# Optimization experiments

Measured on AMD Instinct MI355X. Metric: run time of the kernel, lower is better.

## Reference

```python
import jax, jax.numpy as jnp
import numpy as np

N_NODES = 100000
N_EDGES = 1600000
D = 64
N_LAYERS = 6  # 3 KAN blocks x 2 KANLinear
GRID_SIZE = 5
SPLINE_ORDER = 3
N_COEF = GRID_SIZE + SPLINE_ORDER  # 8


def _grid():
    # uniform B-spline grid on [-1, 1], extended by spline_order on each side
    h = 2.0 / GRID_SIZE
    return (jnp.arange(-SPLINE_ORDER, GRID_SIZE + SPLINE_ORDER + 1, dtype=jnp.float32) * h - 1.0)  # [G+2k+1]=12


def b_splines(x):
    # x: [N, D] -> bases [N, D, G+k] via Cox-de Boor recursion
    grid = _grid()
    xe = x[..., None]  # [N, D, 1]
    b = ((xe >= grid[:-1]) & (xe < grid[1:])).astype(x.dtype)  # order-0, [N,D,G+2k]
    for p in range(1, SPLINE_ORDER + 1):
        left = (xe - grid[: -(p + 1)]) / (grid[p:-1] - grid[: -(p + 1)])
        right = (grid[p + 1:] - xe) / (grid[p + 1:] - grid[1:-p])
        b = left * b[..., :-1] + right * b[..., 1:]
    return b  # [N, D, N_COEF]


def kan_linear(x, bw, sw, ss):
    # efficient-KAN layer: SiLU base branch + B-spline branch with standalone scaler
    base = jax.nn.silu(x) @ bw.T                      # [N, O]
    bas = b_splines(x)                                # [N, D, K]
    spline = jnp.einsum('ndk,odk->no', bas, sw * ss[..., None])
    return base + spline


def spmm(edge_row, edge_col, edge_val, x):
    # out[i] = sum_{(i,j) in E} val * x[j]  -- COO sparse-dense matmul
    msgs = edge_val[:, None] * x[edge_col]            # [E, D] gather
    return jax.ops.segment_sum(msgs, edge_row, num_segments=N_NODES)


def setup_inputs() -> dict:
    key = jax.random.key(0)
    ks = jax.random.split(key, 7)
    x = jax.random.uniform(ks[0], (N_NODES, D), jnp.float32, -1.0, 1.0)
    edge_row = jnp.sort(jax.random.randint(ks[1], (N_EDGES,), 0, N_NODES))
    edge_col = jax.random.randint(ks[2], (N_EDGES,), 0, N_NODES)
    edge_val = jax.random.uniform(ks[3], (N_EDGES,), jnp.float32, 0.0, 1.0) * (1.0 / 16.0)
    base_w = jax.random.normal(ks[4], (N_LAYERS, D, D), jnp.float32) * (1.0 / np.sqrt(D))
    spline_w = jax.random.normal(ks[5], (N_LAYERS, D, D, N_COEF), jnp.float32) * 0.1
    spline_s = jax.random.normal(ks[6], (N_LAYERS, D, D), jnp.float32) * (1.0 / np.sqrt(D))
    return {"x": x, "edge_val": edge_val, "base_w": base_w, "spline_w": spline_w,
            "spline_s": spline_s, "edge_row": edge_row, "edge_col": edge_col}


def reference(x, edge_val, base_w, spline_w, spline_s, edge_row, edge_col):
    idx = 0
    for _block in range(3):          # mp_layers = 3 KAN blocks
        x = spmm(edge_row, edge_col, edge_val, x)
        for _l in range(2):          # kan_layers = 2 KANLinear per block
            x = kan_linear(x, base_w[idx], spline_w[idx], spline_s[idx])
            idx += 1
    return x
```

## Files before the change

kernel.cpp:

```cpp
#include <hip/hip_runtime.h>
#include <math.h>

#define N_NODES 100000
#define N_EDGES 1600000
#define DIM 64
#define N_LAYERS 6
#define N_COEF 8
#define NSTEP 18
#define NTILE 32
#define KAN_BLOCKS (N_NODES / NTILE)

typedef _Float16 f16x8 __attribute__((ext_vector_type(8)));
typedef _Float16 f16x4 __attribute__((ext_vector_type(4)));
typedef float f32x4 __attribute__((ext_vector_type(4)));

__device__ __forceinline__ unsigned f16u(float v) {
    return (unsigned)__builtin_bit_cast(unsigned short, (_Float16)v);
}

__global__ void build_wcf(const float* __restrict__ bw,
                          const float* __restrict__ sw,
                          const float* __restrict__ ss,
                          uint4* __restrict__ wcf) {
    int idx = blockIdx.x * blockDim.x + threadIdx.x;
    if (idx >= N_LAYERS * NSTEP * 4 * 64) return;
    int lane = idx & 63;
    int nt   = (idx >> 6) & 3;
    int s    = (idx >> 8) % NSTEP;
    int l    = idx / (64 * 4 * NSTEP);
    int o = nt * 16 + (lane & 15);

    unsigned short h[8];
#pragma unroll
    for (int j = 0; j < 8; ++j) {
        int k = s * 32 + ((lane >> 4) << 3) + j;
        int d = k / 9;
        int r = k - d * 9;
        float v;
        if (r == 0) v = bw[(l * DIM + o) * DIM + d];
        else        v = sw[((l * DIM + o) * DIM + d) * N_COEF + (r - 1)] *
                        ss[(l * DIM + o) * DIM + d];
        h[j] = __builtin_bit_cast(unsigned short, (_Float16)v);
    }
    uint4 uh;
    uh.x = (unsigned)h[0] | ((unsigned)h[1] << 16);
    uh.y = (unsigned)h[2] | ((unsigned)h[3] << 16);
    uh.z = (unsigned)h[4] | ((unsigned)h[5] << 16);
    uh.w = (unsigned)h[6] | ((unsigned)h[7] << 16);
    wcf[((l * NSTEP + s) * 4 + nt) * 64 + lane] = uh;
}

__global__ void build_rowptr(const int* __restrict__ erow, int* __restrict__ rp) {
    int i = blockIdx.x * blockDim.x + threadIdx.x;
    if (i > N_NODES) return;
    if (i == N_NODES) { rp[i] = N_EDGES; return; }
    int a = 0, b = N_EDGES;
    while (a < b) { int m = (a + b) >> 1; if (erow[m] < i) a = m + 1; else b = m; }
    rp[i] = a;
}

__global__ void conv_f16(const float* __restrict__ in, _Float16* __restrict__ out) {
    int i = blockIdx.x * blockDim.x + threadIdx.x;
    float4 v = *(const float4*)(in + (size_t)i * 4);
    f16x4 h = { (_Float16)v.x, (_Float16)v.y, (_Float16)v.z, (_Float16)v.w };
    *(f16x4*)(out + (size_t)i * 4) = h;
}

#define META16(C, V, BASE)                                              \
    _Pragma("unroll")                                                   \
    for (int i_ = 0; i_ < 4; ++i_) {                                    \
        int e_ = (BASE) + 4 * i_ + q;                                   \
        if (e_ < end) { C[i_] = ecol[e_]; V[i_] = ev[e_]; }             \
        else          { C[i_] = 0;        V[i_] = 0.f; }                \
    }

__global__ __launch_bounds__(256) void spmm_kernel(const int* __restrict__ rp,
                                                   const int* __restrict__ ecol,
                                                   const float* __restrict__ ev,
                                                   const _Float16* __restrict__ x,
                                                   _Float16* __restrict__ y) {
    int wid = (blockIdx.x * blockDim.x + threadIdx.x) >> 6;
    int lane = threadIdx.x & 63;
    if (wid >= N_NODES) return;
    int q = lane >> 4;
    int c16 = lane & 15;
    int e0 = rp[wid], end = rp[wid + 1];

    float4 acc = {0.f, 0.f, 0.f, 0.f};
    int ca[4]; float va[4];
    int cb[4]; float vb[4];
    META16(ca, va, e0)

    for (int eb = e0; eb < end; eb += 16) {
        META16(cb, vb, eb + 16)
        f16x4 g0 = *(const f16x4*)&x[(size_t)ca[0] * DIM + c16 * 4];
        f16x4 g1 = *(const f16x4*)&x[(size_t)ca[1] * DIM + c16 * 4];
        f16x4 g2 = *(const f16x4*)&x[(size_t)ca[2] * DIM + c16 * 4];
        f16x4 g3 = *(const f16x4*)&x[(size_t)ca[3] * DIM + c16 * 4];
        acc.x += va[0] * (float)g0[0]; acc.y += va[0] * (float)g0[1];
        acc.z += va[0] * (float)g0[2]; acc.w += va[0] * (float)g0[3];
        acc.x += va[1] * (float)g1[0]; acc.y += va[1] * (float)g1[1];
        acc.z += va[1] * (float)g1[2]; acc.w += va[1] * (float)g1[3];
        acc.x += va[2] * (float)g2[0]; acc.y += va[2] * (float)g2[1];
        acc.z += va[2] * (float)g2[2]; acc.w += va[2] * (float)g2[3];
        acc.x += va[3] * (float)g3[0]; acc.y += va[3] * (float)g3[1];
        acc.z += va[3] * (float)g3[2]; acc.w += va[3] * (float)g3[3];
#pragma unroll
        for (int i_ = 0; i_ < 4; ++i_) { ca[i_] = cb[i_]; va[i_] = vb[i_]; }
    }

    acc.x += __shfl_xor(acc.x, 16); acc.y += __shfl_xor(acc.y, 16);
    acc.z += __shfl_xor(acc.z, 16); acc.w += __shfl_xor(acc.w, 16);
    acc.x += __shfl_xor(acc.x, 32); acc.y += __shfl_xor(acc.y, 32);
    acc.z += __shfl_xor(acc.z, 32); acc.w += __shfl_xor(acc.w, 32);

    if (lane < 16) {
        f16x4 h = { (_Float16)acc.x, (_Float16)acc.y, (_Float16)acc.z, (_Float16)acc.w };
        *(f16x4*)&y[(size_t)wid * DIM + c16 * 4] = h;
    }
}

__device__ __forceinline__ void spline_window(float xv, unsigned long long& lo,
                                              unsigned long long& hi) {
    float t = xv * 2.5f + 5.5f;
    float fl = floorf(t);
    float u = t - fl;
    int c = (int)fl;
    bool valid = (t >= 0.f) && (t < 11.f);
    float u2 = u * u, u3 = u2 * u, um = 1.f - u;
    const float k6 = 1.f / 6.f;
    float N0 = um * um * um * k6;
    float N1 = (3.f * u3 - 6.f * u2 + 4.f) * k6;
    float N2 = (-3.f * u3 + 3.f * u2 + 3.f * u + 1.f) * k6;
    float N3 = u3 * k6;
    if (!valid) { N0 = 0.f; N1 = 0.f; N2 = 0.f; N3 = 0.f; }
    unsigned n01 = f16u(N0) | (f16u(N1) << 16);
    unsigned n23 = f16u(N2) | (f16u(N3) << 16);
    unsigned long long big = (unsigned long long)n01 | ((unsigned long long)n23 << 32);
    int qb = c - 3;
    qb = qb < -3 ? -3 : (qb > 7 ? 7 : qb);
    int sh = qb * 16;
    lo = 0; hi = 0;
    if (sh >= 0) {
        if (sh < 64) { lo = big << sh; hi = (big >> 1) >> (63 - sh); }
        else         { hi = big << (sh - 64); }
    } else {
        lo = big >> (-sh);
    }
}

__device__ __forceinline__ void feat_pair(char* lds, int lbase, int Xsw, int d,
                                          float xe, float xo) {
    float se_f = xe * __builtin_amdgcn_rcpf(1.f + __expf(-xe));
    float so_f = xo * __builtin_amdgcn_rcpf(1.f + __expf(-xo));
    unsigned se = f16u(se_f), so = f16u(so_f);

    unsigned long long loE, hiE, loO, hiO;
    spline_window(xe, loE, hiE);
    spline_window(xo, loO, hiO);

    unsigned wv[9];
    wv[0] = se | ((unsigned)loE << 16);
    wv[1] = (unsigned)(loE >> 16);
    wv[2] = (unsigned)(loE >> 48) | ((unsigned)hiE << 16);
    wv[3] = (unsigned)(hiE >> 16);
    wv[4] = (unsigned)(hiE >> 48) | (so << 16);
    wv[5] = (unsigned)loO;
    wv[6] = (unsigned)(loO >> 32);
    wv[7] = (unsigned)hiO;
    wv[8] = (unsigned)(hiO >> 32);

    int base = lbase + 18 * d;
#pragma unroll
    for (int j = 0; j < 9; ++j)
        *(unsigned*)(&lds[(base + 4 * j) ^ Xsw]) = wv[j];
}

template<int F32OUT>
__global__ __launch_bounds__(256) void kan_mfma(const _Float16* __restrict__ xin,
                                                const uint4* __restrict__ wl,
                                                void* __restrict__ outp) {
    __shared__ alignas(16) char lds[NTILE * 1152];

    int tid = threadIdx.x;
    int lane = tid & 63;
    int w = tid >> 6;
    int node0 = blockIdx.x * NTILE;

    int fn = tid >> 3;
    int fq = tid & 7;
    int Xsw = (fn & 7) << 4;
    int lbase = fn * 1152;
    {
        const _Float16* xr_ = &xin[(size_t)(node0 + fn) * DIM + fq * 4];
        f16x4 h0 = *(const f16x4*)(xr_);
        f16x4 h1 = *(const f16x4*)(xr_ + 32);
        int d0 = fq * 4;
        feat_pair(lds, lbase, Xsw, d0,          (float)h0[0], (float)h0[1]);
        feat_pair(lds, lbase, Xsw, d0 + 2,      (float)h0[2], (float)h0[3]);
        feat_pair(lds, lbase, Xsw, d0 + 32,     (float)h1[0], (float)h1[1]);
        feat_pair(lds, lbase, Xsw, d0 + 32 + 2, (float)h1[2], (float)h1[3]);
    }
    __syncthreads();

    int row = lane & 15, kg = lane >> 4;
    int xr = (row & 7) << 4;
    int rb0 = row * 1152;
    int rb1 = (16 + row) * 1152;

    f32x4 acc0 = {0.f, 0.f, 0.f, 0.f};
    f32x4 acc1 = {0.f, 0.f, 0.f, 0.f};
#pragma unroll
    for (int s = 0; s < NSTEP; ++s) {
        f16x8 bh = __builtin_bit_cast(f16x8, wl[(s * 4 + w) * 64 + lane]);
        int pofs = ((s * 4 + kg) << 4) ^ xr;
        f16x8 a0 = *(const f16x8*)(&lds[rb0 + pofs]);
        f16x8 a1 = *(const f16x8*)(&lds[rb1 + pofs]);
        acc0 = __builtin_amdgcn_mfma_f32_16x16x32_f16(a0, bh, acc0, 0, 0, 0);
        acc1 = __builtin_amdgcn_mfma_f32_16x16x32_f16(a1, bh, acc1, 0, 0, 0);
    }

    int o = w * 16 + row;
    int rbase = kg * 4;
    if (F32OUT) {
        float* out = (float*)outp;
#pragma unroll
        for (int r = 0; r < 4; ++r) {
            out[(size_t)(node0 + rbase + r) * DIM + o]      = acc0[r];
            out[(size_t)(node0 + 16 + rbase + r) * DIM + o] = acc1[r];
        }
    } else {
        _Float16* out = (_Float16*)outp;
#pragma unroll
        for (int r = 0; r < 4; ++r) {
            out[(size_t)(node0 + rbase + r) * DIM + o]      = (_Float16)acc0[r];
            out[(size_t)(node0 + 16 + rbase + r) * DIM + o] = (_Float16)acc1[r];
        }
    }
}

extern "C" void kernel_launch(void* const* d_in, const int* in_sizes, int n_in,
                              void* d_out, int out_size, void* d_ws, size_t ws_size,
                              hipStream_t stream) {
    const float* x     = (const float*)d_in[0];
    const float* eval_ = (const float*)d_in[1];
    const float* bw    = (const float*)d_in[2];
    const float* sw    = (const float*)d_in[3];
    const float* ss    = (const float*)d_in[4];
    const int*   erow  = (const int*)d_in[5];
    const int*   ecol  = (const int*)d_in[6];
    float* out = (float*)d_out;

    const size_t HB = (size_t)N_NODES * DIM * sizeof(_Float16);
    _Float16* H0 = (_Float16*)d_ws;
    _Float16* H1 = (_Float16*)((char*)d_ws + HB);
    uint4* wcf = (uint4*)((char*)d_ws + 2 * HB);
    int*   rp  = (int*)((char*)d_ws + 2 * HB + 442368);

    const size_t WL = (size_t)NSTEP * 4 * 64;

    build_wcf<<<(N_LAYERS * NSTEP * 4 * 64 + 255) / 256, 256, 0, stream>>>(bw, sw, ss, wcf);
    build_rowptr<<<(N_NODES + 256) / 256, 256, 0, stream>>>(erow, rp);
    conv_f16<<<(N_NODES * DIM / 4 + 255) / 256, 256, 0, stream>>>(x, H0);

    const int SPMM_BLOCKS = N_NODES / 4;

    spmm_kernel<<<SPMM_BLOCKS, 256, 0, stream>>>(rp, ecol, eval_, H0, H1);
    kan_mfma<0><<<KAN_BLOCKS, 256, 0, stream>>>(H1, wcf + 0 * WL, H1);
    kan_mfma<0><<<KAN_BLOCKS, 256, 0, stream>>>(H1, wcf + 1 * WL, H0);

    spmm_kernel<<<SPMM_BLOCKS, 256, 0, stream>>>(rp, ecol, eval_, H0, H1);
    kan_mfma<0><<<KAN_BLOCKS, 256, 0, stream>>>(H1, wcf + 2 * WL, H1);
    kan_mfma<0><<<KAN_BLOCKS, 256, 0, stream>>>(H1, wcf + 3 * WL, H0);

    spmm_kernel<<<SPMM_BLOCKS, 256, 0, stream>>>(rp, ecol, eval_, H0, H1);
    kan_mfma<0><<<KAN_BLOCKS, 256, 0, stream>>>(H1, wcf + 4 * WL, H1);
    kan_mfma<1><<<KAN_BLOCKS, 256, 0, stream>>>(H1, wcf + 5 * WL, out);
}
```

Before: 272.4 us.

## Double KAN node tile to 64, fuse prep kernels, use 32-bit gather indexing

Each KAN MFMA block now processes 64 nodes with four accumulators, so each weight fragment load is reused across more MFMAs, with bounds guards for the partial final tile. The three setup kernels are merged into one launch with block-range dispatch to cut launch overhead. The SpMM gather address is computed with an unsigned 32-bit shift to save 64-bit arithmetic. The larger LDS footprint per block reduces how many blocks can be resident per CU.

```diff
diff --git a/kernel.cpp b/kernel.cpp
--- a/kernel.cpp
+++ b/kernel.cpp
@@ -7,8 +7,12 @@
 #define N_LAYERS 6
 #define N_COEF 8
 #define NSTEP 18
-#define NTILE 32
+#define NTILE 64
 #define KAN_BLOCKS (N_NODES / NTILE)
+
+#define WCF_BLOCKS 108
+#define RP_BLOCKS  391
+#define CONV_BLOCKS 6250
 
 typedef _Float16 f16x8 __attribute__((ext_vector_type(8)));
 typedef _Float16 f16x4 __attribute__((ext_vector_type(4)));
@@ -18,52 +22,53 @@
     return (unsigned)__builtin_bit_cast(unsigned short, (_Float16)v);
 }
 
-__global__ void build_wcf(const float* __restrict__ bw,
-                          const float* __restrict__ sw,
-                          const float* __restrict__ ss,
-                          uint4* __restrict__ wcf) {
-    int idx = blockIdx.x * blockDim.x + threadIdx.x;
-    if (idx >= N_LAYERS * NSTEP * 4 * 64) return;
-    int lane = idx & 63;
-    int nt   = (idx >> 6) & 3;
-    int s    = (idx >> 8) % NSTEP;
-    int l    = idx / (64 * 4 * NSTEP);
-    int o = nt * 16 + (lane & 15);
-
-    unsigned short h[8];
-#pragma unroll
-    for (int j = 0; j < 8; ++j) {
-        int k = s * 32 + ((lane >> 4) << 3) + j;
-        int d = k / 9;
-        int r = k - d * 9;
-        float v;
-        if (r == 0) v = bw[(l * DIM + o) * DIM + d];
-        else        v = sw[((l * DIM + o) * DIM + d) * N_COEF + (r - 1)] *
-                        ss[(l * DIM + o) * DIM + d];
-        h[j] = __builtin_bit_cast(unsigned short, (_Float16)v);
-    }
-    uint4 uh;
-    uh.x = (unsigned)h[0] | ((unsigned)h[1] << 16);
-    uh.y = (unsigned)h[2] | ((unsigned)h[3] << 16);
-    uh.z = (unsigned)h[4] | ((unsigned)h[5] << 16);
-    uh.w = (unsigned)h[6] | ((unsigned)h[7] << 16);
-    wcf[((l * NSTEP + s) * 4 + nt) * 64 + lane] = uh;
-}
-
-__global__ void build_rowptr(const int* __restrict__ erow, int* __restrict__ rp) {
-    int i = blockIdx.x * blockDim.x + threadIdx.x;
-    if (i > N_NODES) return;
-    if (i == N_NODES) { rp[i] = N_EDGES; return; }
-    int a = 0, b = N_EDGES;
-    while (a < b) { int m = (a + b) >> 1; if (erow[m] < i) a = m + 1; else b = m; }
-    rp[i] = a;
-}
-
-__global__ void conv_f16(const float* __restrict__ in, _Float16* __restrict__ out) {
-    int i = blockIdx.x * blockDim.x + threadIdx.x;
-    float4 v = *(const float4*)(in + (size_t)i * 4);
-    f16x4 h = { (_Float16)v.x, (_Float16)v.y, (_Float16)v.z, (_Float16)v.w };
-    *(f16x4*)(out + (size_t)i * 4) = h;
+__global__ __launch_bounds__(256) void prep(const float* __restrict__ bw,
+                                            const float* __restrict__ sw,
+                                            const float* __restrict__ ss,
+                                            uint4* __restrict__ wcf,
+                                            const int* __restrict__ erow,
+                                            int* __restrict__ rp,
+                                            const float* __restrict__ x,
+                                            _Float16* __restrict__ H0) {
+    int bid = blockIdx.x;
+    if (bid < WCF_BLOCKS) {
+        int idx = bid * 256 + threadIdx.x;
+        int lane = idx & 63;
+        int nt   = (idx >> 6) & 3;
+        int s    = (idx >> 8) % NSTEP;
+        int l    = idx / (64 * 4 * NSTEP);
+        int o = nt * 16 + (lane & 15);
+        unsigned short h[8];
+#pragma unroll
+        for (int j = 0; j < 8; ++j) {
+            int k = s * 32 + ((lane >> 4) << 3) + j;
+            int d = k / 9;
+            int r = k - d * 9;
+            float v;
+            if (r == 0) v = bw[(l * DIM + o) * DIM + d];
+            else        v = sw[((l * DIM + o) * DIM + d) * N_COEF + (r - 1)] *
+                            ss[(l * DIM + o) * DIM + d];
+            h[j] = __builtin_bit_cast(unsigned short, (_Float16)v);
+        }
+        uint4 uh;
+        uh.x = (unsigned)h[0] | ((unsigned)h[1] << 16);
+        uh.y = (unsigned)h[2] | ((unsigned)h[3] << 16);
+        uh.z = (unsigned)h[4] | ((unsigned)h[5] << 16);
+        uh.w = (unsigned)h[6] | ((unsigned)h[7] << 16);
+        wcf[((l * NSTEP + s) * 4 + nt) * 64 + lane] = uh;
+    } else if (bid < WCF_BLOCKS + RP_BLOCKS) {
+        int i = (bid - WCF_BLOCKS) * 256 + threadIdx.x;
+        if (i > N_NODES) return;
+        if (i == N_NODES) { rp[i] = N_EDGES; return; }
+        int a = 0, b = N_EDGES;
+        while (a < b) { int m = (a + b) >> 1; if (erow[m] < i) a = m + 1; else b = m; }
+        rp[i] = a;
+    } else {
+        int i = (bid - WCF_BLOCKS - RP_BLOCKS) * 256 + threadIdx.x;
+        float4 v = *(const float4*)(x + (size_t)i * 4);
+        f16x4 h = { (_Float16)v.x, (_Float16)v.y, (_Float16)v.z, (_Float16)v.w };
+        *(f16x4*)(H0 + (size_t)i * 4) = h;
+    }
 }
 
 #define META16(C, V, BASE)                                              \
@@ -93,10 +98,10 @@
 
     for (int eb = e0; eb < end; eb += 16) {
         META16(cb, vb, eb + 16)
-        f16x4 g0 = *(const f16x4*)&x[(size_t)ca[0] * DIM + c16 * 4];
-        f16x4 g1 = *(const f16x4*)&x[(size_t)ca[1] * DIM + c16 * 4];
-        f16x4 g2 = *(const f16x4*)&x[(size_t)ca[2] * DIM + c16 * 4];
-        f16x4 g3 = *(const f16x4*)&x[(size_t)ca[3] * DIM + c16 * 4];
+        f16x4 g0 = *(const f16x4*)&x[((unsigned)ca[0] << 6) + c16 * 4];
+        f16x4 g1 = *(const f16x4*)&x[((unsigned)ca[1] << 6) + c16 * 4];
+        f16x4 g2 = *(const f16x4*)&x[((unsigned)ca[2] << 6) + c16 * 4];
+        f16x4 g3 = *(const f16x4*)&x[((unsigned)ca[3] << 6) + c16 * 4];
         acc.x += va[0] * (float)g0[0]; acc.y += va[0] * (float)g0[1];
         acc.z += va[0] * (float)g0[2]; acc.w += va[0] * (float)g0[3];
         acc.x += va[1] * (float)g1[0]; acc.y += va[1] * (float)g1[1];
@@ -187,54 +192,65 @@
     int w = tid >> 6;
     int node0 = blockIdx.x * NTILE;
 
-    int fn = tid >> 3;
-    int fq = tid & 7;
+    int fn = tid >> 2;
+    int fq = tid & 3;
+    bool live = (node0 + fn) < N_NODES;
     int Xsw = (fn & 7) << 4;
     int lbase = fn * 1152;
-    {
+    if (live) {
         const _Float16* xr_ = &xin[(size_t)(node0 + fn) * DIM + fq * 4];
-        f16x4 h0 = *(const f16x4*)(xr_);
-        f16x4 h1 = *(const f16x4*)(xr_ + 32);
-        int d0 = fq * 4;
-        feat_pair(lds, lbase, Xsw, d0,          (float)h0[0], (float)h0[1]);
-        feat_pair(lds, lbase, Xsw, d0 + 2,      (float)h0[2], (float)h0[3]);
-        feat_pair(lds, lbase, Xsw, d0 + 32,     (float)h1[0], (float)h1[1]);
-        feat_pair(lds, lbase, Xsw, d0 + 32 + 2, (float)h1[2], (float)h1[3]);
+#pragma unroll
+        for (int i = 0; i < 4; ++i) {
+            f16x4 h = *(const f16x4*)(xr_ + i * 16);
+            int d0 = fq * 4 + i * 16;
+            feat_pair(lds, lbase, Xsw, d0,     (float)h[0], (float)h[1]);
+            feat_pair(lds, lbase, Xsw, d0 + 2, (float)h[2], (float)h[3]);
+        }
     }
     __syncthreads();
 
     int row = lane & 15, kg = lane >> 4;
     int xr = (row & 7) << 4;
-    int rb0 = row * 1152;
-    int rb1 = (16 + row) * 1152;
+    int rb0 = (0 * 16 + row) * 1152;
+    int rb1 = (1 * 16 + row) * 1152;
+    int rb2 = (2 * 16 + row) * 1152;
+    int rb3 = (3 * 16 + row) * 1152;
 
     f32x4 acc0 = {0.f, 0.f, 0.f, 0.f};
     f32x4 acc1 = {0.f, 0.f, 0.f, 0.f};
+    f32x4 acc2 = {0.f, 0.f, 0.f, 0.f};
+    f32x4 acc3 = {0.f, 0.f, 0.f, 0.f};
 #pragma unroll
     for (int s = 0; s < NSTEP; ++s) {
         f16x8 bh = __builtin_bit_cast(f16x8, wl[(s * 4 + w) * 64 + lane]);
         int pofs = ((s * 4 + kg) << 4) ^ xr;
         f16x8 a0 = *(const f16x8*)(&lds[rb0 + pofs]);
         f16x8 a1 = *(const f16x8*)(&lds[rb1 + pofs]);
+        f16x8 a2 = *(const f16x8*)(&lds[rb2 + pofs]);
+        f16x8 a3 = *(const f16x8*)(&lds[rb3 + pofs]);
         acc0 = __builtin_amdgcn_mfma_f32_16x16x32_f16(a0, bh, acc0, 0, 0, 0);
         acc1 = __builtin_amdgcn_mfma_f32_16x16x32_f16(a1, bh, acc1, 0, 0, 0);
+        acc2 = __builtin_amdgcn_mfma_f32_16x16x32_f16(a2, bh, acc2, 0, 0, 0);
+        acc3 = __builtin_amdgcn_mfma_f32_16x16x32_f16(a3, bh, acc3, 0, 0, 0);
     }
 
     int o = w * 16 + row;
     int rbase = kg * 4;
-    if (F32OUT) {
-        float* out = (float*)outp;
-#pragma unroll
-        for (int r = 0; r < 4; ++r) {
-            out[(size_t)(node0 + rbase + r) * DIM + o]      = acc0[r];
-            out[(size_t)(node0 + 16 + rbase + r) * DIM + o] = acc1[r];
-        }
-    } else {
-        _Float16* out = (_Float16*)outp;
-#pragma unroll
-        for (int r = 0; r < 4; ++r) {
-            out[(size_t)(node0 + rbase + r) * DIM + o]      = (_Float16)acc0[r];
-            out[(size_t)(node0 + 16 + rbase + r) * DIM + o] = (_Float16)acc1[r];
+#pragma unroll
+    for (int m = 0; m < 4; ++m) {
+        f32x4 acc = m == 0 ? acc0 : m == 1 ? acc1 : m == 2 ? acc2 : acc3;
+        int nb = node0 + m * 16 + rbase;
+        if (nb >= N_NODES) continue;
+        if (F32OUT) {
+            float* out = (float*)outp;
+#pragma unroll
+            for (int r = 0; r < 4; ++r)
+                out[(size_t)(nb + r) * DIM + o] = acc[r];
+        } else {
+            _Float16* out = (_Float16*)outp;
+#pragma unroll
+            for (int r = 0; r < 4; ++r)
+                out[(size_t)(nb + r) * DIM + o] = (_Float16)acc[r];
         }
     }
 }
@@ -258,22 +274,22 @@
     int*   rp  = (int*)((char*)d_ws + 2 * HB + 442368);
 
     const size_t WL = (size_t)NSTEP * 4 * 64;
-
-    build_wcf<<<(N_LAYERS * NSTEP * 4 * 64 + 255) / 256, 256, 0, stream>>>(bw, sw, ss, wcf);
-    build_rowptr<<<(N_NODES + 256) / 256, 256, 0, stream>>>(erow, rp);
-    conv_f16<<<(N_NODES * DIM / 4 + 255) / 256, 256, 0, stream>>>(x, H0);
+    const int KB = (N_NODES + NTILE - 1) / NTILE;
+
+    prep<<<WCF_BLOCKS + RP_BLOCKS + CONV_BLOCKS, 256, 0, stream>>>(
+        bw, sw, ss, wcf, erow, rp, x, H0);
 
     const int SPMM_BLOCKS = N_NODES / 4;
 
     spmm_kernel<<<SPMM_BLOCKS, 256, 0, stream>>>(rp, ecol, eval_, H0, H1);
-    kan_mfma<0><<<KAN_BLOCKS, 256, 0, stream>>>(H1, wcf + 0 * WL, H1);
-    kan_mfma<0><<<KAN_BLOCKS, 256, 0, stream>>>(H1, wcf + 1 * WL, H0);
+    kan_mfma<0><<<KB, 256, 0, stream>>>(H1, wcf + 0 * WL, H1);
+    kan_mfma<0><<<KB, 256, 0, stream>>>(H1, wcf + 1 * WL, H0);
 
     spmm_kernel<<<SPMM_BLOCKS, 256, 0, stream>>>(rp, ecol, eval_, H0, H1);
-    kan_mfma<0><<<KAN_BLOCKS, 256, 0, stream>>>(H1, wcf + 2 * WL, H1);
-    kan_mfma<0><<<KAN_BLOCKS, 256, 0, stream>>>(H1, wcf + 3 * WL, H0);
+    kan_mfma<0><<<KB, 256, 0, stream>>>(H1, wcf + 2 * WL, H1);
+    kan_mfma<0><<<KB, 256, 0, stream>>>(H1, wcf + 3 * WL, H0);
 
     spmm_kernel<<<SPMM_BLOCKS, 256, 0, stream>>>(rp, ecol, eval_, H0, H1);
-    kan_mfma<0><<<KAN_BLOCKS, 256, 0, stream>>>(H1, wcf + 4 * WL, H1);
-    kan_mfma<1><<<KAN_BLOCKS, 256, 0, stream>>>(H1, wcf + 5 * WL, out);
-}
+    kan_mfma<0><<<KB, 256, 0, stream>>>(H1, wcf + 4 * WL, H1);
+    kan_mfma<1><<<KB, 256, 0, stream>>>(H1, wcf + 5 * WL, out);
+}
```

New measurement: 295.8 us. 1.09x slower.

## Fuse paired KAN layers into one kernel and merge prep kernels

Applied to the files above, without the earlier changes.

Each pair of consecutive KANLinear layers now runs in one kernel. The intermediate activations stay in LDS, where they are re-featurized for the second layer's MFMA loop, so the global round trip and one launch per block are removed. The three setup kernels are merged into a single prep launch with a block-range dispatch. The SpMM gather index arithmetic also switches to 32-bit shifts. The cost is extra syncthreads and LDS reuse inside the fused kernel.

```diff
diff --git a/kernel.cpp b/kernel.cpp
--- a/kernel.cpp
+++ b/kernel.cpp
@@ -9,6 +9,11 @@
 #define NSTEP 18
 #define NTILE 32
 #define KAN_BLOCKS (N_NODES / NTILE)
+#define C1S 68
+
+#define WCF_BLOCKS 108
+#define RP_BLOCKS  391
+#define CONV_BLOCKS 6250
 
 typedef _Float16 f16x8 __attribute__((ext_vector_type(8)));
 typedef _Float16 f16x4 __attribute__((ext_vector_type(4)));
@@ -18,52 +23,53 @@
     return (unsigned)__builtin_bit_cast(unsigned short, (_Float16)v);
 }
 
-__global__ void build_wcf(const float* __restrict__ bw,
-                          const float* __restrict__ sw,
-                          const float* __restrict__ ss,
-                          uint4* __restrict__ wcf) {
-    int idx = blockIdx.x * blockDim.x + threadIdx.x;
-    if (idx >= N_LAYERS * NSTEP * 4 * 64) return;
-    int lane = idx & 63;
-    int nt   = (idx >> 6) & 3;
-    int s    = (idx >> 8) % NSTEP;
-    int l    = idx / (64 * 4 * NSTEP);
-    int o = nt * 16 + (lane & 15);
-
-    unsigned short h[8];
-#pragma unroll
-    for (int j = 0; j < 8; ++j) {
-        int k = s * 32 + ((lane >> 4) << 3) + j;
-        int d = k / 9;
-        int r = k - d * 9;
-        float v;
-        if (r == 0) v = bw[(l * DIM + o) * DIM + d];
-        else        v = sw[((l * DIM + o) * DIM + d) * N_COEF + (r - 1)] *
-                        ss[(l * DIM + o) * DIM + d];
-        h[j] = __builtin_bit_cast(unsigned short, (_Float16)v);
-    }
-    uint4 uh;
-    uh.x = (unsigned)h[0] | ((unsigned)h[1] << 16);
-    uh.y = (unsigned)h[2] | ((unsigned)h[3] << 16);
-    uh.z = (unsigned)h[4] | ((unsigned)h[5] << 16);
-    uh.w = (unsigned)h[6] | ((unsigned)h[7] << 16);
-    wcf[((l * NSTEP + s) * 4 + nt) * 64 + lane] = uh;
-}
-
-__global__ void build_rowptr(const int* __restrict__ erow, int* __restrict__ rp) {
-    int i = blockIdx.x * blockDim.x + threadIdx.x;
-    if (i > N_NODES) return;
-    if (i == N_NODES) { rp[i] = N_EDGES; return; }
-    int a = 0, b = N_EDGES;
-    while (a < b) { int m = (a + b) >> 1; if (erow[m] < i) a = m + 1; else b = m; }
-    rp[i] = a;
-}
-
-__global__ void conv_f16(const float* __restrict__ in, _Float16* __restrict__ out) {
-    int i = blockIdx.x * blockDim.x + threadIdx.x;
-    float4 v = *(const float4*)(in + (size_t)i * 4);
-    f16x4 h = { (_Float16)v.x, (_Float16)v.y, (_Float16)v.z, (_Float16)v.w };
-    *(f16x4*)(out + (size_t)i * 4) = h;
+__global__ __launch_bounds__(256) void prep(const float* __restrict__ bw,
+                                            const float* __restrict__ sw,
+                                            const float* __restrict__ ss,
+                                            uint4* __restrict__ wcf,
+                                            const int* __restrict__ erow,
+                                            int* __restrict__ rp,
+                                            const float* __restrict__ x,
+                                            _Float16* __restrict__ H0) {
+    int bid = blockIdx.x;
+    if (bid < WCF_BLOCKS) {
+        int idx = bid * 256 + threadIdx.x;
+        int lane = idx & 63;
+        int nt   = (idx >> 6) & 3;
+        int s    = (idx >> 8) % NSTEP;
+        int l    = idx / (64 * 4 * NSTEP);
+        int o = nt * 16 + (lane & 15);
+        unsigned short h[8];
+#pragma unroll
+        for (int j = 0; j < 8; ++j) {
+            int k = s * 32 + ((lane >> 4) << 3) + j;
+            int d = k / 9;
+            int r = k - d * 9;
+            float v;
+            if (r == 0) v = bw[(l * DIM + o) * DIM + d];
+            else        v = sw[((l * DIM + o) * DIM + d) * N_COEF + (r - 1)] *
+                            ss[(l * DIM + o) * DIM + d];
+            h[j] = __builtin_bit_cast(unsigned short, (_Float16)v);
+        }
+        uint4 uh;
+        uh.x = (unsigned)h[0] | ((unsigned)h[1] << 16);
+        uh.y = (unsigned)h[2] | ((unsigned)h[3] << 16);
+        uh.z = (unsigned)h[4] | ((unsigned)h[5] << 16);
+        uh.w = (unsigned)h[6] | ((unsigned)h[7] << 16);
+        wcf[((l * NSTEP + s) * 4 + nt) * 64 + lane] = uh;
+    } else if (bid < WCF_BLOCKS + RP_BLOCKS) {
+        int i = (bid - WCF_BLOCKS) * 256 + threadIdx.x;
+        if (i > N_NODES) return;
+        if (i == N_NODES) { rp[i] = N_EDGES; return; }
+        int a = 0, b = N_EDGES;
+        while (a < b) { int m = (a + b) >> 1; if (erow[m] < i) a = m + 1; else b = m; }
+        rp[i] = a;
+    } else {
+        int i = (bid - WCF_BLOCKS - RP_BLOCKS) * 256 + threadIdx.x;
+        float4 v = *(const float4*)(x + (size_t)i * 4);
+        f16x4 h = { (_Float16)v.x, (_Float16)v.y, (_Float16)v.z, (_Float16)v.w };
+        *(f16x4*)(H0 + (size_t)i * 4) = h;
+    }
 }
 
 #define META16(C, V, BASE)                                              \
@@ -93,10 +99,10 @@
 
     for (int eb = e0; eb < end; eb += 16) {
         META16(cb, vb, eb + 16)
-        f16x4 g0 = *(const f16x4*)&x[(size_t)ca[0] * DIM + c16 * 4];
-        f16x4 g1 = *(const f16x4*)&x[(size_t)ca[1] * DIM + c16 * 4];
-        f16x4 g2 = *(const f16x4*)&x[(size_t)ca[2] * DIM + c16 * 4];
-        f16x4 g3 = *(const f16x4*)&x[(size_t)ca[3] * DIM + c16 * 4];
+        f16x4 g0 = *(const f16x4*)&x[((unsigned)ca[0] << 6) + c16 * 4];
+        f16x4 g1 = *(const f16x4*)&x[((unsigned)ca[1] << 6) + c16 * 4];
+        f16x4 g2 = *(const f16x4*)&x[((unsigned)ca[2] << 6) + c16 * 4];
+        f16x4 g3 = *(const f16x4*)&x[((unsigned)ca[3] << 6) + c16 * 4];
         acc.x += va[0] * (float)g0[0]; acc.y += va[0] * (float)g0[1];
         acc.z += va[0] * (float)g0[2]; acc.w += va[0] * (float)g0[3];
         acc.x += va[1] * (float)g1[0]; acc.y += va[1] * (float)g1[1];
@@ -177,10 +183,12 @@
 }
 
 template<int F32OUT>
-__global__ __launch_bounds__(256) void kan_mfma(const _Float16* __restrict__ xin,
-                                                const uint4* __restrict__ wl,
-                                                void* __restrict__ outp) {
+__global__ __launch_bounds__(256) void kan2_mfma(const _Float16* __restrict__ xin,
+                                                 const uint4* __restrict__ wlA,
+                                                 const uint4* __restrict__ wlB,
+                                                 void* __restrict__ outp) {
     __shared__ alignas(16) char lds[NTILE * 1152];
+    _Float16* c1 = (_Float16*)lds;
 
     int tid = threadIdx.x;
     int lane = tid & 63;
@@ -191,6 +199,13 @@
     int fq = tid & 7;
     int Xsw = (fn & 7) << 4;
     int lbase = fn * 1152;
+    int row = lane & 15, kg = lane >> 4;
+    int xr = (row & 7) << 4;
+    int rb0 = row * 1152;
+    int rb1 = (16 + row) * 1152;
+    int o = w * 16 + row;
+    int rbase = kg * 4;
+
     {
         const _Float16* xr_ = &xin[(size_t)(node0 + fn) * DIM + fq * 4];
         f16x4 h0 = *(const f16x4*)(xr_);
@@ -203,25 +218,51 @@
     }
     __syncthreads();
 
-    int row = lane & 15, kg = lane >> 4;
-    int xr = (row & 7) << 4;
-    int rb0 = row * 1152;
-    int rb1 = (16 + row) * 1152;
-
     f32x4 acc0 = {0.f, 0.f, 0.f, 0.f};
     f32x4 acc1 = {0.f, 0.f, 0.f, 0.f};
 #pragma unroll
     for (int s = 0; s < NSTEP; ++s) {
-        f16x8 bh = __builtin_bit_cast(f16x8, wl[(s * 4 + w) * 64 + lane]);
+        f16x8 bh = __builtin_bit_cast(f16x8, wlA[(s * 4 + w) * 64 + lane]);
         int pofs = ((s * 4 + kg) << 4) ^ xr;
         f16x8 a0 = *(const f16x8*)(&lds[rb0 + pofs]);
         f16x8 a1 = *(const f16x8*)(&lds[rb1 + pofs]);
         acc0 = __builtin_amdgcn_mfma_f32_16x16x32_f16(a0, bh, acc0, 0, 0, 0);
         acc1 = __builtin_amdgcn_mfma_f32_16x16x32_f16(a1, bh, acc1, 0, 0, 0);
     }
-
-    int o = w * 16 + row;
-    int rbase = kg * 4;
+    __syncthreads();
+
+#pragma unroll
+    for (int r = 0; r < 4; ++r) {
+        c1[(rbase + r) * C1S + o]      = (_Float16)acc0[r];
+        c1[(16 + rbase + r) * C1S + o] = (_Float16)acc1[r];
+    }
+    __syncthreads();
+
+    f16x4 g0 = *(const f16x4*)&c1[fn * C1S + fq * 4];
+    f16x4 g1 = *(const f16x4*)&c1[fn * C1S + fq * 4 + 32];
+    __syncthreads();
+
+    {
+        int d0 = fq * 4;
+        feat_pair(lds, lbase, Xsw, d0,          (float)g0[0], (float)g0[1]);
+        feat_pair(lds, lbase, Xsw, d0 + 2,      (float)g0[2], (float)g0[3]);
+        feat_pair(lds, lbase, Xsw, d0 + 32,     (float)g1[0], (float)g1[1]);
+        feat_pair(lds, lbase, Xsw, d0 + 32 + 2, (float)g1[2], (float)g1[3]);
+    }
+    __syncthreads();
+
+    acc0 = (f32x4){0.f, 0.f, 0.f, 0.f};
+    acc1 = (f32x4){0.f, 0.f, 0.f, 0.f};
+#pragma unroll
+    for (int s = 0; s < NSTEP; ++s) {
+        f16x8 bh = __builtin_bit_cast(f16x8, wlB[(s * 4 + w) * 64 + lane]);
+        int pofs = ((s * 4 + kg) << 4) ^ xr;
+        f16x8 a0 = *(const f16x8*)(&lds[rb0 + pofs]);
+        f16x8 a1 = *(const f16x8*)(&lds[rb1 + pofs]);
+        acc0 = __builtin_amdgcn_mfma_f32_16x16x32_f16(a0, bh, acc0, 0, 0, 0);
+        acc1 = __builtin_amdgcn_mfma_f32_16x16x32_f16(a1, bh, acc1, 0, 0, 0);
+    }
+
     if (F32OUT) {
         float* out = (float*)outp;
 #pragma unroll
@@ -259,21 +300,17 @@
 
     const size_t WL = (size_t)NSTEP * 4 * 64;
 
-    build_wcf<<<(N_LAYERS * NSTEP * 4 * 64 + 255) / 256, 256, 0, stream>>>(bw, sw, ss, wcf);
-    build_rowptr<<<(N_NODES + 256) / 256, 256, 0, stream>>>(erow, rp);
-    conv_f16<<<(N_NODES * DIM / 4 + 255) / 256, 256, 0, stream>>>(x, H0);
+    prep<<<WCF_BLOCKS + RP_BLOCKS + CONV_BLOCKS, 256, 0, stream>>>(
+        bw, sw, ss, wcf, erow, rp, x, H0);
 
     const int SPMM_BLOCKS = N_NODES / 4;
 
     spmm_kernel<<<SPMM_BLOCKS, 256, 0, stream>>>(rp, ecol, eval_, H0, H1);
-    kan_mfma<0><<<KAN_BLOCKS, 256, 0, stream>>>(H1, wcf + 0 * WL, H1);
-    kan_mfma<0><<<KAN_BLOCKS, 256, 0, stream>>>(H1, wcf + 1 * WL, H0);
+    kan2_mfma<0><<<KAN_BLOCKS, 256, 0, stream>>>(H1, wcf + 0 * WL, wcf + 1 * WL, H0);
 
     spmm_kernel<<<SPMM_BLOCKS, 256, 0, stream>>>(rp, ecol, eval_, H0, H1);
-    kan_mfma<0><<<KAN_BLOCKS, 256, 0, stream>>>(H1, wcf + 2 * WL, H1);
-    kan_mfma<0><<<KAN_BLOCKS, 256, 0, stream>>>(H1, wcf + 3 * WL, H0);
+    kan2_mfma<0><<<KAN_BLOCKS, 256, 0, stream>>>(H1, wcf + 2 * WL, wcf + 3 * WL, H0);
 
     spmm_kernel<<<SPMM_BLOCKS, 256, 0, stream>>>(rp, ecol, eval_, H0, H1);
-    kan_mfma<0><<<KAN_BLOCKS, 256, 0, stream>>>(H1, wcf + 4 * WL, H1);
-    kan_mfma<1><<<KAN_BLOCKS, 256, 0, stream>>>(H1, wcf + 5 * WL, out);
-}
+    kan2_mfma<1><<<KAN_BLOCKS, 256, 0, stream>>>(H1, wcf + 4 * WL, wcf + 5 * WL, out);
+}
```

Measured after the change: 241.0 us. 1.13x faster.
